# Kernel optimization log

Measured on AMD Instinct MI355X. Metric: run time of the kernel, lower is better.

Reference implementation:

```python
import jax, jax.numpy as jnp
import numpy as np

B = 16
T_LEN, T_DIM = 149, 768
H = W = 56
S_DIM = 512
EPS = 1e-5


def setup_inputs() -> dict:
    key = jax.random.key(0)
    ks = jax.random.split(key, 12)
    N = H * W  # 3136
    return {
        "x": jax.random.normal(ks[0], (B, T_LEN, T_DIM), dtype=jnp.float32),
        "y": jax.random.normal(ks[1], (B, S_DIM, H, W), dtype=jnp.float32),
        # Conv1d(time_len -> h*w, k=1)
        "W_conv1": jax.random.normal(ks[2], (N, T_LEN), dtype=jnp.float32) * (1.0 / np.sqrt(T_LEN)),
        "b_conv1": jnp.zeros((N,), dtype=jnp.float32),
        # LayerNorms
        "ln1_g": jnp.ones((T_DIM,), dtype=jnp.float32),
        "ln1_b": jnp.zeros((T_DIM,), dtype=jnp.float32),
        "ln2_g": jnp.ones((S_DIM,), dtype=jnp.float32),
        "ln2_b": jnp.zeros((S_DIM,), dtype=jnp.float32),
        # positional encodings (1, C, H, W)
        "pe_wave": jax.random.normal(ks[3], (1, T_DIM, H, W), dtype=jnp.float32) * 0.02,
        "pe_spec": jax.random.normal(ks[4], (1, S_DIM, H, W), dtype=jnp.float32) * 0.02,
        # CrossAttention2D 1x1 convs
        "Wq": jax.random.normal(ks[5], (S_DIM, T_DIM), dtype=jnp.float32) * (1.0 / np.sqrt(T_DIM)),
        "bq": jnp.zeros((S_DIM,), dtype=jnp.float32),
        "Wk": jax.random.normal(ks[6], (S_DIM, S_DIM), dtype=jnp.float32) * (1.0 / np.sqrt(S_DIM)),
        "bk": jnp.zeros((S_DIM,), dtype=jnp.float32),
    }


def _layernorm(t, g, b):
    # t: (..., C), normalized over last axis
    m = jnp.mean(t, axis=-1, keepdims=True)
    v = jnp.mean(jnp.square(t - m), axis=-1, keepdims=True)
    return (t - m) * jax.lax.rsqrt(v + EPS) * g + b


def reference(x, y, W_conv1, b_conv1, ln1_g, ln1_b, ln2_g, ln2_b,
              pe_wave, pe_spec, Wq, bq, Wk, bk):
    # conv1d k=1 over channel dim time_len: (B,149,768) -> (B,3136,768)
    xe = jnp.einsum('bld,ol->bod', x, W_conv1) + b_conv1[None, :, None]
    # rearrange 'b (h w) c -> b h w c' (channel-last for LN/attention)
    nx = xe.reshape(x.shape[0], H, W, T_DIM)
    nx = _layernorm(nx, ln1_g, ln1_b) + pe_wave.transpose(0, 2, 3, 1)  # (B,H,W,768)

    ny = y.transpose(0, 2, 3, 1)  # (B,H,W,512)
    ny = _layernorm(ny, ln2_g, ln2_b) + pe_spec.transpose(0, 2, 3, 1)

    # 1x1 convs -> q, k; value is norm_y itself
    q = jnp.einsum('bhwc,oc->bhwo', nx, Wq) + bq  # (B,H,W,512)
    k = jnp.einsum('bhwc,oc->bhwo', ny, Wk) + bk  # (B,H,W,512)
    v = ny

    # row-local attention: each (b,h) row of W=56 tokens attends within itself
    scores = jnp.einsum('bhqc,bhkc->bhqk', q, k) / jnp.sqrt(jnp.float32(S_DIM))
    attn = jax.nn.softmax(scores, axis=-1)  # (B,H,W,W)
    out = jnp.einsum('bhqk,bhkc->bhqc', attn, v)  # (B,H,W,512)

    # permute back to (B,C,H,W), residual add
    return out.transpose(0, 3, 1, 2) + y
```

## Files before the change

kernel.cpp:

```cpp
#include <hip/hip_runtime.h>
#include <hip/hip_bf16.h>
#include <math.h>

typedef short bf16x8 __attribute__((ext_vector_type(8)));
typedef float f32x4 __attribute__((ext_vector_type(4)));

#define LN_EPS 1e-5f

static __device__ __forceinline__ float b2f(unsigned short u){
  unsigned int x = ((unsigned int)u) << 16; float f; __builtin_memcpy(&f,&x,4); return f;
}
static __device__ __forceinline__ unsigned short f2b(float f){
  unsigned int x; __builtin_memcpy(&x,&f,4);
  x += 0x7fffu + ((x>>16)&1u);
  return (unsigned short)(x>>16);
}

static __device__ __forceinline__ void gload_lds16(const void* g, void* l){
  __builtin_amdgcn_global_load_lds(
      (const __attribute__((address_space(1))) unsigned int*)g,
      (__attribute__((address_space(3))) unsigned int*)l, 16, 0, 0);
}

#define MFMA16(a,b,c) __builtin_amdgcn_mfma_f32_16x16x32_bf16(a,b,c,0,0,0)

__global__ void pack_rowpad(const float* __restrict__ src, unsigned short* __restrict__ dst,
                            int rows, int srcK, int dstK, int rowsPad){
  int idx = blockIdx.x*256 + threadIdx.x;
  if (idx >= rowsPad*dstK) return;
  int r = idx / dstK, kk = idx - r*dstK;
  float v = (r < rows && kk < srcK) ? src[(size_t)r*srcK + kk] : 0.f;
  dst[idx] = f2b(v);
}

__global__ __launch_bounds__(256) void pack_xt(const float* __restrict__ x, unsigned short* __restrict__ xt){
  __shared__ float tile[32][33];
  int b = blockIdx.z;
  int l0 = blockIdx.y*32, d0 = blockIdx.x*32;
  int tl = threadIdx.x & 31, tw = threadIdx.x >> 5;
  for (int r=0;r<32;r+=8){
    int l = l0 + tw + r;
    tile[tw+r][tl] = (l<149) ? x[((size_t)b*149 + l)*768 + d0 + tl] : 0.f;
  }
  __syncthreads();
  for (int r=0;r<32;r+=8){
    int d = d0 + tw + r;
    int l = l0 + tl;
    if (l < 160) xt[((size_t)b*768 + d)*160 + l] = f2b(tile[tl][tw+r]);
  }
}

__global__ __launch_bounds__(256) void transpose_pe(const float* __restrict__ src, float* __restrict__ dst, int C){
  __shared__ float tile[32][33];
  int c0 = blockIdx.y*32, o0 = blockIdx.x*32;
  int tl = threadIdx.x & 31, tw = threadIdx.x >> 5;
  for (int r=0;r<32;r+=8)
    tile[tw+r][tl] = src[(size_t)(c0+tw+r)*3136 + o0 + tl];
  __syncthreads();
  for (int r=0;r<32;r+=8)
    dst[(size_t)(o0+tw+r)*C + c0 + tl] = tile[tl][tw+r];
}

__global__ __launch_bounds__(256)
void conv160(const unsigned short* __restrict__ A, const unsigned short* __restrict__ Bt,
             unsigned short* __restrict__ C, int M, int N,
             long long bStride, long long cStride){
  __shared__ __align__(16) unsigned short lds[40960];
  const int K = 160;
  int tid = threadIdx.x;
  int lane = tid & 63, wave = tid >> 6;
  int wm = (wave >> 1)*64, wn = (wave & 1)*64;
  int lr = lane & 15, lo = lane >> 4;
  int m0 = blockIdx.x*128, n0 = blockIdx.y*128;
  const unsigned short* Bb = Bt + (size_t)blockIdx.z*bStride;
  unsigned short* Cb = C + (size_t)blockIdx.z*cStride;

  #pragma unroll
  for (int i=0;i<20;i++){
    int cbase = i*256 + wave*64;
    int tensor = (cbase >= 2560) ? 1 : 0;
    int ccb = cbase - tensor*2560;
    int cc = ccb + lane;
    int r = cc / 20, pc = cc - r*20;
    int sw = (r ^ (r >> 2)) & 3;
    int ps = pc ^ sw;
    const unsigned short* srcT = tensor ? (Bb + (size_t)n0*K) : (A + (size_t)m0*K);
    gload_lds16(srcT + (size_t)r*K + ps*8, lds + tensor*20480 + ccb*8);
  }
  asm volatile("s_waitcnt vmcnt(0)" ::: "memory");
  __builtin_amdgcn_s_barrier();

  f32x4 acc[4][4];
  #pragma unroll
  for (int i=0;i<4;i++)
    #pragma unroll
    for (int j=0;j<4;j++) acc[i][j]=(f32x4){0.f,0.f,0.f,0.f};
  #pragma unroll
  for (int kk=0; kk<5; ++kk){
    bf16x8 af[4], bfr[4];
    #pragma unroll
    for (int mi=0;mi<4;mi++){
      int row = wm + mi*16 + lr;
      int p = kk*4 + (lo ^ ((row ^ (row>>2)) & 3));
      af[mi] = *reinterpret_cast<const bf16x8*>(&lds[row*160 + p*8]);
    }
    #pragma unroll
    for (int nj=0;nj<4;nj++){
      int row = wn + nj*16 + lr;
      int p = kk*4 + (lo ^ ((row ^ (row>>2)) & 3));
      bfr[nj] = *reinterpret_cast<const bf16x8*>(&lds[20480 + row*160 + p*8]);
    }
    #pragma unroll
    for (int mi=0;mi<4;mi++)
      #pragma unroll
      for (int nj=0;nj<4;nj++)
        acc[mi][nj] = MFMA16(af[mi], bfr[nj], acc[mi][nj]);
  }
  int er = lo*4;
  #pragma unroll
  for (int mi=0;mi<4;mi++)
    #pragma unroll
    for (int nj=0;nj<4;nj++){
      int col = n0 + wn + nj*16 + lr;
      #pragma unroll
      for (int e=0;e<4;e++){
        int row = m0 + wm + mi*16 + er + e;
        if (row < M) Cb[(size_t)row*N + col] = f2b(acc[mi][nj][e]);
      }
    }
}

__global__ __launch_bounds__(512)
void gemm256_dual_bk32(const unsigned short* __restrict__ A0, const unsigned short* __restrict__ Bt0,
                       unsigned short* __restrict__ C0, const float* __restrict__ bias0, int K0,
                       const unsigned short* __restrict__ A1, const unsigned short* __restrict__ Bt1,
                       unsigned short* __restrict__ C1, const float* __restrict__ bias1, int K1,
                       int M, int N){
  __shared__ __align__(16) unsigned short lds[32768];
  int tid = threadIdx.x;
  int lane = tid & 63, wave = tid >> 6;
  int wr = wave >> 2, wc = wave & 3;
  int lr = lane & 15, lo = lane >> 4;
  int cpx = gridDim.x >> 3;
  int id = blockIdx.x;
  int sid = (id & 7)*cpx + (id >> 3);
  int q_sel = sid & 1;
  int s2 = sid >> 1;
  const unsigned short* A; const unsigned short* Bt; unsigned short* C;
  const float* bias; int K;
  if (q_sel == 0){ A=A0; Bt=Bt0; C=C0; bias=bias0; K=K0; }
  else           { A=A1; Bt=Bt1; C=C1; bias=bias1; K=K1; }
  int nby = N >> 8;
  int bx = s2 / nby, by = s2 - bx*nby;
  int m0 = bx << 8, n0 = by << 8;
  int NT = K >> 5;

  f32x4 acc[8][4];
  #pragma unroll
  for (int i=0;i<8;i++)
    #pragma unroll
    for (int j=0;j<4;j++) acc[i][j]=(f32x4){0.f,0.f,0.f,0.f};

  auto STAGE = [&](int t){
    if (t >= NT) return;
    int buf = t & 1;
    int k0 = t << 5;
    #pragma unroll
    for (int i=0;i<4;i++){
      int cbase = i*512 + wave*64;
      int tensor = cbase >> 10;
      int ccb = cbase & 1023;
      int cc = ccb + lane;
      int r = cc >> 2, pc = cc & 3;
      int ps = pc ^ ((r ^ (r >> 2)) & 3);
      const unsigned short* srcT = tensor ? (Bt + (size_t)n0*K) : (A + (size_t)m0*K);
      gload_lds16(srcT + (size_t)r*K + k0 + ps*8, lds + buf*16384 + tensor*8192 + ccb*8);
    }
  };
  auto rdA = [&](int buf, int mi)->bf16x8{
    int row = wr*128 + mi*16 + lr;
    int p = lo ^ ((row ^ (row >> 2)) & 3);
    return *reinterpret_cast<const bf16x8*>(&lds[buf*16384 + row*32 + p*8]);
  };
  auto rdB = [&](int buf, int nj)->bf16x8{
    int row = wc*64 + nj*16 + lr;
    int p = lo ^ ((row ^ (row >> 2)) & 3);
    return *reinterpret_cast<const bf16x8*>(&lds[buf*16384 + 8192 + row*32 + p*8]);
  };

  STAGE(0);
  asm volatile("s_waitcnt vmcnt(0)" ::: "memory");
  __builtin_amdgcn_s_barrier();

  for (int t=0; t<NT; ++t){
    int buf = t & 1;
    STAGE(t+1);
    bf16x8 bfr[4], af[4];
    #pragma unroll
    for (int nj=0;nj<4;nj++) bfr[nj] = rdB(buf,nj);
    #pragma unroll
    for (int i=0;i<4;i++) af[i] = rdA(buf,i);
    asm volatile("s_waitcnt lgkmcnt(0)" ::: "memory");
    __builtin_amdgcn_sched_barrier(0);
    __builtin_amdgcn_s_setprio(1);
    #pragma unroll
    for (int i=0;i<4;i++)
      #pragma unroll
      for (int nj=0;nj<4;nj++)
        acc[i][nj] = MFMA16(af[i], bfr[nj], acc[i][nj]);
    __builtin_amdgcn_s_setprio(0);
    #pragma unroll
    for (int i=0;i<4;i++) af[i] = rdA(buf,4+i);
    asm volatile("s_waitcnt lgkmcnt(0)" ::: "memory");
    __builtin_amdgcn_sched_barrier(0);
    __builtin_amdgcn_s_setprio(1);
    #pragma unroll
    for (int i=0;i<4;i++)
      #pragma unroll
      for (int nj=0;nj<4;nj++)
        acc[4+i][nj] = MFMA16(af[i], bfr[nj], acc[4+i][nj]);
    __builtin_amdgcn_s_setprio(0);
    asm volatile("s_waitcnt vmcnt(0)" ::: "memory");
    __builtin_amdgcn_s_barrier();
  }

  int er = lo*4;
  #pragma unroll
  for (int nj=0;nj<4;nj++){
    int col = n0 + wc*64 + nj*16 + lr;
    float bv = bias ? bias[col] : 0.f;
    #pragma unroll
    for (int mi=0;mi<8;mi++){
      int row = m0 + wr*128 + mi*16 + er;
      #pragma unroll
      for (int e=0;e<4;e++)
        C[(size_t)(row+e)*N + col] = f2b(acc[mi][nj][e] + bv);
    }
  }
}

__global__ __launch_bounds__(256) void ln1_kernel(unsigned short* __restrict__ xe,
    const float* __restrict__ g, const float* __restrict__ be, const float* __restrict__ pet){
  int b = blockIdx.y;
  int o0 = blockIdx.x*8;
  int t = threadIdx.x;
  int lane = t & 63, wv = t >> 6;
  __shared__ float ws1[8][4], ws2[8][4];
  __shared__ float mArr[8], rArr[8];
  float vals[8][3];
  #pragma unroll
  for (int oi=0;oi<8;oi++){
    size_t base = ((size_t)b*3136 + o0 + oi)*768;
    #pragma unroll
    for (int j=0;j<3;j++) vals[oi][j] = b2f(xe[base + t + 256*j]);
  }
  #pragma unroll
  for (int oi=0;oi<8;oi++){
    float s1=0.f, s2=0.f;
    #pragma unroll
    for (int j=0;j<3;j++){ float v=vals[oi][j]; s1+=v; s2+=v*v; }
    #pragma unroll
    for (int d=32; d>0; d>>=1){ s1 += __shfl_xor(s1,d); s2 += __shfl_xor(s2,d); }
    if (lane==0){ ws1[oi][wv]=s1; ws2[oi][wv]=s2; }
  }
  __syncthreads();
  if (t < 8){
    float a = ws1[t][0]+ws1[t][1]+ws1[t][2]+ws1[t][3];
    float c = ws2[t][0]+ws2[t][1]+ws2[t][2]+ws2[t][3];
    float m = a*(1.f/768.f);
    float var = c*(1.f/768.f) - m*m;
    mArr[t] = m; rArr[t] = rsqrtf(var + LN_EPS);
  }
  __syncthreads();
  #pragma unroll
  for (int oi=0;oi<8;oi++){
    size_t base = ((size_t)b*3136 + o0 + oi)*768;
    size_t pb = (size_t)(o0+oi)*768;
    float m=mArr[oi], r=rArr[oi];
    #pragma unroll
    for (int j=0;j<3;j++){
      int d = t + 256*j;
      xe[base+d] = f2b((vals[oi][j]-m)*r*g[d] + be[d] + pet[pb+d]);
    }
  }
}

__global__ __launch_bounds__(256) void ln2_kernel(const float* __restrict__ y,
    unsigned short* __restrict__ ny, unsigned short* __restrict__ nyT,
    const float* __restrict__ g, const float* __restrict__ bb, const float* __restrict__ pe){
  int b = blockIdx.y;
  int o0 = blockIdx.x*32;
  int t = threadIdx.x;
  int oi = t & 31, cg = t >> 5;
  __shared__ float red1[8][33], red2[8][33];
  __shared__ float mArr[32], rArr[32];
  __shared__ unsigned short tile[32][520];
  size_t ybase = (size_t)b*512*3136 + o0;
  float vals[64];
  float s1=0.f, s2=0.f;
  #pragma unroll
  for (int ci=0; ci<64; ci++){
    int c = cg*64 + ci;
    float v = y[ybase + (size_t)c*3136 + oi];
    vals[ci] = v;
    s1 += v; s2 += v*v;
  }
  red1[cg][oi]=s1; red2[cg][oi]=s2;
  __syncthreads();
  if (t < 32){
    float a=0.f, c2=0.f;
    #pragma unroll
    for (int kk=0;kk<8;kk++){ a+=red1[kk][t]; c2+=red2[kk][t]; }
    float m=a*(1.f/512.f);
    float var=c2*(1.f/512.f)-m*m;
    mArr[t]=m; rArr[t]=rsqrtf(var+LN_EPS);
  }
  __syncthreads();
  float m = mArr[oi], r = rArr[oi];
  #pragma unroll
  for (int ci=0; ci<64; ci++){
    int c = cg*64 + ci;
    float v = (vals[ci]-m)*r*g[c] + bb[c] + pe[(size_t)c*3136 + o0 + oi];
    tile[oi][c] = f2b(v);
  }
  __syncthreads();
  size_t nybase = ((size_t)b*3136 + o0)*512;
  for (int p = t; p < 32*64; p += 256){
    int oo = p >> 6, cp = (p & 63)*8;
    *reinterpret_cast<uint4*>(ny + nybase + (size_t)oo*512 + cp) =
        *reinterpret_cast<const uint4*>(&tile[oo][cp]);
  }
  for (int c2 = t; c2 < 512; c2 += 256){
    unsigned short row[32];
    #pragma unroll
    for (int o=0;o<32;o++) row[o] = tile[o][c2];
    size_t a = ((size_t)b*512 + c2)*3136 + o0;
    #pragma unroll
    for (int u=0;u<4;u++)
      *reinterpret_cast<uint4*>(nyT + a + u*8) = *reinterpret_cast<const uint4*>(&row[u*8]);
  }
}

__global__ __launch_bounds__(512) void attn_kernel(const unsigned short* __restrict__ q,
    const unsigned short* __restrict__ k, const unsigned short* __restrict__ vT,
    const float* __restrict__ y, float* __restrict__ outp){
  int id = blockIdx.x;
  int sid = (id & 7)*112 + (id >> 3);
  int b = sid / 56, h = sid - b*56;
  int tid = threadIdx.x;
  int lane = tid & 63, w = tid >> 6;
  int wc = w & 3, wk = w >> 2;
  size_t base = (size_t)b*3136 + (size_t)h*56;
  __shared__ __align__(16) float SfP[2][56][60];
  __shared__ __align__(16) unsigned short Sb[64*64];

  f32x4 acc[4];
  #pragma unroll
  for (int mi=0;mi<4;mi++) acc[mi]=(f32x4){0.f,0.f,0.f,0.f};
  int lr = lane & 15, lo = lane >> 4;
  int lk = lo*8;
  int kr = wc*16 + lr; if (kr > 55) kr = 55;
  const unsigned short* krow = k + (base + kr)*512 + wk*256;
  const unsigned short* qrow = q + base*512 + wk*256;
  #pragma unroll
  for (int k0=0;k0<256;k0+=32){
    bf16x8 kf = *reinterpret_cast<const bf16x8*>(krow + k0 + lk);
    #pragma unroll
    for (int mi=0;mi<4;mi++){
      int qr = mi*16 + lr; if (qr > 55) qr = 55;
      bf16x8 qf = *reinterpret_cast<const bf16x8*>(qrow + (size_t)qr*512 + k0 + lk);
      acc[mi] = __builtin_amdgcn_mfma_f32_16x16x32_bf16(qf, kf, acc[mi], 0,0,0);
    }
  }

  const unsigned short* vb = vT + (size_t)b*512*3136 + (size_t)h*56;
  bf16x8 vfr[2][2][2];
  #pragma unroll
  for (int hp=0; hp<2; ++hp)
    #pragma unroll
    for (int kt=0;kt<2;++kt)
      #pragma unroll
      for (int mi=0;mi<2;++mi){
        int d = w*64 + hp*32 + mi*16 + lr;
        vfr[hp][kt][mi] = *reinterpret_cast<const bf16x8*>(vb + (size_t)d*3136 + kt*32 + lk);
      }

  int col = wc*16 + lr;
  int er = lo*4;
  if (col < 56){
    #pragma unroll
    for (int mi=0;mi<4;mi++)
      #pragma unroll
      for (int e=0;e<4;e++){
        int row = mi*16 + er + e;
        if (row < 56) SfP[wk][row][col] = acc[mi][e];
      }
  }
  __syncthreads();

  const float scale = 0.04419417382415922f;
  for (int r=0;r<7;r++){
    int i = w*7 + r;
    float xv = (lane<56) ? (SfP[0][i][lane] + SfP[1][i][lane])*scale : -1e30f;
    float mx = xv;
    #pragma unroll
    for (int d=32; d>0; d>>=1) mx = fmaxf(mx, __shfl_xor(mx,d));
    float ev = (lane<56) ? __expf(xv-mx) : 0.f;
    float sm = ev;
    #pragma unroll
    for (int d=32; d>0; d>>=1) sm += __shfl_xor(sm,d);
    unsigned short pv = (lane<56) ? f2b(ev/sm) : (unsigned short)0;
    int bo = i*128 + ((lane*2) ^ ((i&7)<<4));
    *reinterpret_cast<unsigned short*>(reinterpret_cast<char*>(Sb) + bo) = pv;
  }
  __syncthreads();

  bf16x8 pf[2][4];
  #pragma unroll
  for (int kt=0;kt<2;++kt)
    #pragma unroll
    for (int nj=0;nj<4;++nj){
      int row = nj*16 + lr;
      int bo = row*128 + (((kt*64) + lo*16) ^ ((row&7)<<4));
      pf[kt][nj] = *reinterpret_cast<const bf16x8*>(reinterpret_cast<const char*>(Sb) + bo);
    }

  #pragma unroll
  for (int hp=0; hp<2; ++hp){
    f32x4 a2[2][4];
    #pragma unroll
    for (int mi=0;mi<2;mi++)
      #pragma unroll
      for (int nj=0;nj<4;nj++) a2[mi][nj]=(f32x4){0.f,0.f,0.f,0.f};
    #pragma unroll
    for (int kt=0;kt<2;++kt)
      #pragma unroll
      for (int mi=0;mi<2;++mi)
        #pragma unroll
        for (int nj=0;nj<4;++nj)
          a2[mi][nj] = __builtin_amdgcn_mfma_f32_16x16x32_bf16(vfr[hp][kt][mi], pf[kt][nj], a2[mi][nj], 0,0,0);
    #pragma unroll
    for (int mi=0;mi<2;++mi)
      #pragma unroll
      for (int e=0;e<4;++e){
        size_t rowb = ((size_t)b*512 + w*64 + hp*32 + mi*16 + er + e)*3136 + (size_t)h*56;
        #pragma unroll
        for (int nj=0;nj<4;++nj){
          int r = nj*16 + lr;
          if (r < 56) outp[rowb + r] = a2[mi][nj][e] + y[rowb + r];
        }
      }
  }
}

extern "C" void kernel_launch(void* const* d_in, const int* in_sizes, int n_in,
                              void* d_out, int out_size, void* d_ws, size_t ws_size,
                              hipStream_t stream){
  const float* x   = (const float*)d_in[0];
  const float* y   = (const float*)d_in[1];
  const float* Wc  = (const float*)d_in[2];
  const float* g1  = (const float*)d_in[4];
  const float* be1 = (const float*)d_in[5];
  const float* g2  = (const float*)d_in[6];
  const float* be2 = (const float*)d_in[7];
  const float* peW = (const float*)d_in[8];
  const float* peS = (const float*)d_in[9];
  const float* Wq  = (const float*)d_in[10];
  const float* bq  = (const float*)d_in[11];
  const float* Wk  = (const float*)d_in[12];
  const float* bk  = (const float*)d_in[13];
  float* outp = (float*)d_out;

  char* p = (char*)d_ws;
  auto alloc = [&](size_t bytes)->char*{ char* r = p; p += (bytes + 255) & ~(size_t)255; return r; };
  unsigned short* WcB = (unsigned short*)alloc((size_t)3200*160*2);
  unsigned short* xt  = (unsigned short*)alloc((size_t)16*768*160*2);
  unsigned short* WqB = (unsigned short*)alloc((size_t)512*768*2);
  unsigned short* WkB = (unsigned short*)alloc((size_t)512*512*2);
  float* peWt = (float*)alloc((size_t)3136*768*4);
  unsigned short* xe  = (unsigned short*)alloc((size_t)16*3136*768*2);
  unsigned short* ny  = (unsigned short*)alloc((size_t)16*3136*512*2);
  unsigned short* nyT = (unsigned short*)alloc((size_t)16*512*3136*2 + 256);
  unsigned short* qb  = (unsigned short*)alloc((size_t)16*3136*512*2);
  unsigned short* kb  = (unsigned short*)alloc((size_t)16*3136*512*2);

  pack_rowpad<<<dim3((3200*160+255)/256), 256, 0, stream>>>(Wc, WcB, 3136, 149, 160, 3200);
  pack_rowpad<<<dim3((512*768+255)/256), 256, 0, stream>>>(Wq, WqB, 512, 768, 768, 512);
  pack_rowpad<<<dim3((512*512+255)/256), 256, 0, stream>>>(Wk, WkB, 512, 512, 512, 512);
  pack_xt<<<dim3(24,5,16), 256, 0, stream>>>(x, xt);
  transpose_pe<<<dim3(98,24), 256, 0, stream>>>(peW, peWt, 768);

  conv160<<<dim3(25,6,16), 256, 0, stream>>>(WcB, xt, xe, 3136, 768,
                                             768LL*160LL, 3136LL*768LL);
  ln1_kernel<<<dim3(392,16), 256, 0, stream>>>(xe, g1, be1, peWt);
  ln2_kernel<<<dim3(98,16), 256, 0, stream>>>(y, ny, nyT, g2, be2, peS);
  gemm256_dual_bk32<<<dim3(784), 512, 0, stream>>>(xe, WqB, qb, bq, 768,
                                                   ny, WkB, kb, bk, 512, 50176, 512);
  attn_kernel<<<dim3(896), 512, 0, stream>>>(qb, kb, nyT, y, outp);
}
```

Measured before the change: 377.3 us.

## Deepen dual Q/K GEMM to BK=64 with quarter-staged loads interleaved with MFMA

The fused Q/K projection GEMM moves from a K-tile of 32 to 64, which doubles LDS to 128KB of double-buffered tiles and switches to an 8-way XOR swizzle on 128-byte rows. Global-to-LDS loads for the next tile are split into four quarters and issued between the four MFMA phases, each fenced by barriers and partial vmcnt waits. This is meant to halve the number of loop iterations and barrier/wait overhead per K and to hide load latency behind compute. The cost is extra barriers within each iteration and higher LDS use, which may limit occupancy to one block per CU.

New measurement: 363.4 us. -3.7%, faster.

```diff
diff --git a/kernel.cpp b/kernel.cpp
--- a/kernel.cpp
+++ b/kernel.cpp
@@ -131,12 +131,12 @@
 }
 
 __global__ __launch_bounds__(512)
-void gemm256_dual_bk32(const unsigned short* __restrict__ A0, const unsigned short* __restrict__ Bt0,
-                       unsigned short* __restrict__ C0, const float* __restrict__ bias0, int K0,
-                       const unsigned short* __restrict__ A1, const unsigned short* __restrict__ Bt1,
-                       unsigned short* __restrict__ C1, const float* __restrict__ bias1, int K1,
-                       int M, int N){
-  __shared__ __align__(16) unsigned short lds[32768];
+void gemm256_dual(const unsigned short* __restrict__ A0, const unsigned short* __restrict__ Bt0,
+                  unsigned short* __restrict__ C0, const float* __restrict__ bias0, int K0,
+                  const unsigned short* __restrict__ A1, const unsigned short* __restrict__ Bt1,
+                  unsigned short* __restrict__ C1, const float* __restrict__ bias1, int K1,
+                  int M, int N){
+  __shared__ __align__(16) unsigned short lds[65536];
   int tid = threadIdx.x;
   int lane = tid & 63, wave = tid >> 6;
   int wr = wave >> 2, wc = wave & 3;
@@ -153,7 +153,7 @@
   int nby = N >> 8;
   int bx = s2 / nby, by = s2 - bx*nby;
   int m0 = bx << 8, n0 = by << 8;
-  int NT = K >> 5;
+  int NT = K >> 6;
 
   f32x4 acc[8][4];
   #pragma unroll
@@ -161,66 +161,107 @@
     #pragma unroll
     for (int j=0;j<4;j++) acc[i][j]=(f32x4){0.f,0.f,0.f,0.f};
 
-  auto STAGE = [&](int t){
+  auto STAGE = [&](int t, int h){
     if (t >= NT) return;
-    int buf = t & 1;
-    int k0 = t << 5;
-    #pragma unroll
-    for (int i=0;i<4;i++){
-      int cbase = i*512 + wave*64;
-      int tensor = cbase >> 10;
-      int ccb = cbase & 1023;
-      int cc = ccb + lane;
-      int r = cc >> 2, pc = cc & 3;
-      int ps = pc ^ ((r ^ (r >> 2)) & 3);
-      const unsigned short* srcT = tensor ? (Bt + (size_t)n0*K) : (A + (size_t)m0*K);
-      gload_lds16(srcT + (size_t)r*K + k0 + ps*8, lds + buf*16384 + tensor*8192 + ccb*8);
+    int buf = t & 1, tensor = h >> 1, hh = h & 1;
+    int k0 = t << 6;
+    unsigned short* dstbase = lds + buf*32768 + tensor*16384;
+    const unsigned short* srcT = tensor ? (Bt + (size_t)n0*K) : (A + (size_t)m0*K);
+    #pragma unroll
+    for (int ldi=0; ldi<2; ldi++){
+      int c = hh*1024 + ldi*512 + tid;
+      int r = c >> 3;
+      int l = (c & 7) ^ (r & 7);
+      gload_lds16(srcT + (size_t)r*K + k0 + l*8,
+                  dstbase + (hh*1024 + ldi*512 + (wave<<6))*8);
     }
   };
-  auto rdA = [&](int buf, int mi)->bf16x8{
-    int row = wr*128 + mi*16 + lr;
-    int p = lo ^ ((row ^ (row >> 2)) & 3);
-    return *reinterpret_cast<const bf16x8*>(&lds[buf*16384 + row*32 + p*8]);
+  const char* ldsc = reinterpret_cast<const char*>(lds);
+  int swz = lr & 7;
+  auto rdA = [&](int buf, int mi, int kk)->bf16x8{
+    int off = buf*65536 + (wr*128 + mi*16 + lr)*128 + (((kk*4+lo) ^ swz)*16);
+    return *reinterpret_cast<const bf16x8*>(ldsc + off);
   };
-  auto rdB = [&](int buf, int nj)->bf16x8{
-    int row = wc*64 + nj*16 + lr;
-    int p = lo ^ ((row ^ (row >> 2)) & 3);
-    return *reinterpret_cast<const bf16x8*>(&lds[buf*16384 + 8192 + row*32 + p*8]);
+  auto rdB = [&](int buf, int nj, int kk)->bf16x8{
+    int off = buf*65536 + 32768 + (wc*64 + nj*16 + lr)*128 + (((kk*4+lo) ^ swz)*16);
+    return *reinterpret_cast<const bf16x8*>(ldsc + off);
   };
 
-  STAGE(0);
-  asm volatile("s_waitcnt vmcnt(0)" ::: "memory");
+  STAGE(0,0); STAGE(0,1); STAGE(0,2); STAGE(0,3); STAGE(1,0);
+  asm volatile("s_waitcnt vmcnt(2)" ::: "memory");
   __builtin_amdgcn_s_barrier();
 
   for (int t=0; t<NT; ++t){
     int buf = t & 1;
-    STAGE(t+1);
-    bf16x8 bfr[4], af[4];
-    #pragma unroll
-    for (int nj=0;nj<4;nj++) bfr[nj] = rdB(buf,nj);
-    #pragma unroll
-    for (int i=0;i<4;i++) af[i] = rdA(buf,i);
+    bf16x8 bf_[4][2], a0_[2][2], a1_[2][2];
+    #pragma unroll
+    for (int nj=0;nj<4;nj++){ bf_[nj][0]=rdB(buf,nj,0); bf_[nj][1]=rdB(buf,nj,1); }
+    #pragma unroll
+    for (int i=0;i<2;i++){ a0_[i][0]=rdA(buf,i,0);   a0_[i][1]=rdA(buf,i,1); }
+    #pragma unroll
+    for (int i=0;i<2;i++){ a1_[i][0]=rdA(buf,2+i,0); a1_[i][1]=rdA(buf,2+i,1); }
+    STAGE(t+1, 1);
+    __builtin_amdgcn_s_barrier();
     asm volatile("s_waitcnt lgkmcnt(0)" ::: "memory");
     __builtin_amdgcn_sched_barrier(0);
     __builtin_amdgcn_s_setprio(1);
     #pragma unroll
-    for (int i=0;i<4;i++)
-      #pragma unroll
-      for (int nj=0;nj<4;nj++)
-        acc[i][nj] = MFMA16(af[i], bfr[nj], acc[i][nj]);
+    for (int i=0;i<2;i++)
+      #pragma unroll
+      for (int nj=0;nj<4;nj++){
+        acc[i][nj] = MFMA16(a0_[i][0], bf_[nj][0], acc[i][nj]);
+        acc[i][nj] = MFMA16(a0_[i][1], bf_[nj][1], acc[i][nj]);
+      }
     __builtin_amdgcn_s_setprio(0);
-    #pragma unroll
-    for (int i=0;i<4;i++) af[i] = rdA(buf,4+i);
+    __builtin_amdgcn_s_barrier();
+    #pragma unroll
+    for (int i=0;i<2;i++){ a0_[i][0]=rdA(buf,4+i,0); a0_[i][1]=rdA(buf,4+i,1); }
+    STAGE(t+1, 2);
+    __builtin_amdgcn_s_barrier();
     asm volatile("s_waitcnt lgkmcnt(0)" ::: "memory");
     __builtin_amdgcn_sched_barrier(0);
     __builtin_amdgcn_s_setprio(1);
     #pragma unroll
-    for (int i=0;i<4;i++)
-      #pragma unroll
-      for (int nj=0;nj<4;nj++)
-        acc[4+i][nj] = MFMA16(af[i], bfr[nj], acc[4+i][nj]);
+    for (int i=0;i<2;i++)
+      #pragma unroll
+      for (int nj=0;nj<4;nj++){
+        acc[2+i][nj] = MFMA16(a1_[i][0], bf_[nj][0], acc[2+i][nj]);
+        acc[2+i][nj] = MFMA16(a1_[i][1], bf_[nj][1], acc[2+i][nj]);
+      }
     __builtin_amdgcn_s_setprio(0);
-    asm volatile("s_waitcnt vmcnt(0)" ::: "memory");
+    __builtin_amdgcn_s_barrier();
+    #pragma unroll
+    for (int i=0;i<2;i++){ a1_[i][0]=rdA(buf,6+i,0); a1_[i][1]=rdA(buf,6+i,1); }
+    STAGE(t+1, 3);
+    __builtin_amdgcn_s_barrier();
+    asm volatile("s_waitcnt lgkmcnt(0)" ::: "memory");
+    __builtin_amdgcn_sched_barrier(0);
+    __builtin_amdgcn_s_setprio(1);
+    #pragma unroll
+    for (int i=0;i<2;i++)
+      #pragma unroll
+      for (int nj=0;nj<4;nj++){
+        acc[4+i][nj] = MFMA16(a0_[i][0], bf_[nj][0], acc[4+i][nj]);
+        acc[4+i][nj] = MFMA16(a0_[i][1], bf_[nj][1], acc[4+i][nj]);
+      }
+    __builtin_amdgcn_s_setprio(0);
+    __builtin_amdgcn_s_barrier();
+    STAGE(t+2, 0);
+    if (t < NT-2){
+      asm volatile("s_waitcnt vmcnt(2)" ::: "memory");
+    } else {
+      asm volatile("s_waitcnt vmcnt(0)" ::: "memory");
+    }
+    __builtin_amdgcn_s_barrier();
+    __builtin_amdgcn_s_setprio(1);
+    #pragma unroll
+    for (int i=0;i<2;i++)
+      #pragma unroll
+      for (int nj=0;nj<4;nj++){
+        acc[6+i][nj] = MFMA16(a1_[i][0], bf_[nj][0], acc[6+i][nj]);
+        acc[6+i][nj] = MFMA16(a1_[i][1], bf_[nj][1], acc[6+i][nj]);
+      }
+    __builtin_amdgcn_s_setprio(0);
     __builtin_amdgcn_s_barrier();
   }
 
@@ -494,7 +535,7 @@
                                              768LL*160LL, 3136LL*768LL);
   ln1_kernel<<<dim3(392,16), 256, 0, stream>>>(xe, g1, be1, peWt);
   ln2_kernel<<<dim3(98,16), 256, 0, stream>>>(y, ny, nyT, g2, be2, peS);
-  gemm256_dual_bk32<<<dim3(784), 512, 0, stream>>>(xe, WqB, qb, bq, 768,
-                                                   ny, WkB, kb, bk, 512, 50176, 512);
+  gemm256_dual<<<dim3(784), 512, 0, stream>>>(xe, WqB, qb, bq, 768,
+                                              ny, WkB, kb, bk, 512, 50176, 512);
   attn_kernel<<<dim3(896), 512, 0, stream>>>(qb, kb, nyT, y, outp);
 }
```
